# Kernel optimization log

Measured on AMD Instinct MI355X. Metric: run time of the kernel, lower is better.

## Reference

```python
import jax, jax.numpy as jnp
import numpy as np

N_NODES = 100000
N_EDGES = 1600000
IN_DIM = 256
OUT_DIM = 128
EPS = 1e-12  # torch F.normalize default eps


def setup_inputs() -> dict:
    key = jax.random.key(0)
    k1, k2, k3, k4, k5 = jax.random.split(key, 5)
    x = jax.random.normal(k1, (N_NODES, IN_DIM), dtype=jnp.float32)
    edge_index = jax.random.randint(k2, (2, N_EDGES), 0, N_NODES, dtype=jnp.int64)
    # projection (no bias): weight [out, in]
    Wp = jax.random.normal(k3, (OUT_DIM, IN_DIM), dtype=jnp.float32) * 0.05
    # GCNConv internal linear weight [out, out] and output bias [out]
    Wg = jax.random.normal(k4, (OUT_DIM, OUT_DIM), dtype=jnp.float32) * 0.05
    bg = jax.random.normal(k5, (OUT_DIM,), dtype=jnp.float32) * 0.01
    return {"x": x, "edge_index": edge_index, "Wp": Wp, "Wg": Wg, "bg": bg}


def reference(x, edge_index, Wp, Wg, bg):
    n = x.shape[0]
    # projection: x @ Wp^T
    h = x @ Wp.T                      # [N, OUT]
    # GCNConv: transform first, then propagate
    h = h @ Wg.T                      # [N, OUT]
    # add self-loops
    loops = jnp.arange(n, dtype=edge_index.dtype)
    row = jnp.concatenate([edge_index[0], loops])   # source
    col = jnp.concatenate([edge_index[1], loops])   # target
    # symmetric normalization: deg over target index (edge_weight = 1)
    deg = jax.ops.segment_sum(jnp.ones_like(col, dtype=h.dtype), col, num_segments=n)
    dinv = jnp.where(deg > 0, jax.lax.rsqrt(deg), 0.0)
    norm = dinv[row] * dinv[col]                     # [E+N]
    # gather messages from source, scale, scatter-add to target
    msg = h[row] * norm[:, None]                     # [E+N, OUT]
    out = jax.ops.segment_sum(msg, col, num_segments=n)  # [N, OUT]
    out = out + bg
    # F.normalize(dim=1): divide by L2 norm clamped at eps
    nrm = jnp.sqrt(jnp.sum(out * out, axis=1, keepdims=True))
    out = out / jnp.maximum(nrm, EPS)
    return out
```

## Files before the change

### kernel.cpp

```cpp
#include <hip/hip_runtime.h>
#include <hip/hip_fp16.h>

#define NDIM 128
#define KDIM 256
#define MT 5
#define AROW 264
#define CHUNK 3200
#define BSH 8
#define BMASK 255
#define MAXBUCK 400
#define FTH 512

typedef _Float16 half8 __attribute__((ext_vector_type(8)));
typedef _Float16 half4v __attribute__((ext_vector_type(4)));
typedef _Float16 half2v __attribute__((ext_vector_type(2)));
typedef float float4v __attribute__((ext_vector_type(4)));

#if __has_builtin(__builtin_amdgcn_fdot2)
#define HAS_FDOT2 1
#else
#define HAS_FDOT2 0
#endif

__global__ void k_combine_w(const float* __restrict__ Wp, const float* __restrict__ Wg,
                            _Float16* __restrict__ Bfrag) {
    int o = blockIdx.x;
    int i = threadIdx.x;
    float acc = 0.f;
#pragma unroll 4
    for (int k = 0; k < 128; ++k) acc = fmaf(Wg[o * 128 + k], Wp[k * 256 + i], acc);
    int kk = i >> 5, r = i & 31, quad = r >> 3, j = r & 7;
    int ntile = o >> 4, lanen = o & 15, lane = quad * 16 + lanen;
    Bfrag[(((ntile * 8 + kk) * 64) + lane) * 8 + j] = (_Float16)acc;
}

__global__ __launch_bounds__(256) void k_phase1(const int* __restrict__ col, int E,
                                                int* __restrict__ hist, int NBLK, int NBUCK) {
    __shared__ int h[MAXBUCK];
    int tid = threadIdx.x;
    for (int b = tid; b < MAXBUCK; b += 256) h[b] = 0;
    __syncthreads();
    int e0 = blockIdx.x * CHUNK;
    int e1 = min(e0 + CHUNK, E);
    for (int e = e0 + tid; e < e1; e += 256) atomicAdd(&h[col[e] >> BSH], 1);
    __syncthreads();
    for (int b = tid; b < NBUCK; b += 256) hist[b * NBLK + blockIdx.x] = h[b];
}

__global__ __launch_bounds__(1024) void k_scan_blk(int* __restrict__ a, int n,
                                                   int* __restrict__ blockSum) {
    __shared__ int s[1024];
    int t = threadIdx.x;
    int i = blockIdx.x * 1024 + t;
    int v = (i < n) ? a[i] : 0;
    s[t] = v;
    __syncthreads();
    for (int d = 1; d < 1024; d <<= 1) {
        int y = (t >= d) ? s[t - d] : 0;
        __syncthreads();
        s[t] += y;
        __syncthreads();
    }
    if (i < n) a[i] = s[t] - v;
    if (t == 1023) blockSum[blockIdx.x] = s[t];
}

__global__ __launch_bounds__(1024) void k_scan_top(int* __restrict__ blockSum, int nb) {
    __shared__ int s[1024];
    int t = threadIdx.x;
    int v = (t < nb) ? blockSum[t] : 0;
    s[t] = v;
    __syncthreads();
    for (int d = 1; d < 1024; d <<= 1) {
        int y = (t >= d) ? s[t - d] : 0;
        __syncthreads();
        s[t] += y;
        __syncthreads();
    }
    if (t < nb) blockSum[t] = s[t] - v;
}

__global__ __launch_bounds__(256) void k_scan_add(int* __restrict__ a,
                                                  const int* __restrict__ blockOff, int n) {
    int i = blockIdx.x * 256 + threadIdx.x;
    if (i < n) a[i] += blockOff[i >> 10];
}

__global__ __launch_bounds__(256) void k_phase3(const int* __restrict__ ei, int E,
                                                const int* __restrict__ offs, int NBLK, int NBUCK,
                                                int* __restrict__ tmp) {
    __shared__ int cur[MAXBUCK];
    int tid = threadIdx.x;
    for (int b = tid; b < NBUCK; b += 256) cur[b] = offs[b * NBLK + blockIdx.x];
    __syncthreads();
    int e0 = blockIdx.x * CHUNK;
    int e1 = min(e0 + CHUNK, E);
    for (int e = e0 + tid; e < e1; e += 256) {
        int r = ei[e];
        int c = ei[E + e];
        int p = atomicAdd(&cur[c >> BSH], 1);
        tmp[p] = (r << BSH) | (c & BMASK);
    }
}

__global__ __launch_bounds__(FTH) void k_fine(const int* __restrict__ tmp,
                                              const int* __restrict__ offs, int NBLK, int NBUCK,
                                              int N, int E,
                                              int* __restrict__ sortedRow,
                                              int* __restrict__ cnt,
                                              int* __restrict__ rowStart) {
    __shared__ int scnt[256];
    __shared__ int cur[256];
    int b = blockIdx.x;
    int t = threadIdx.x;
    int start = offs[b * NBLK];
    int end = (b + 1 < NBUCK) ? offs[(b + 1) * NBLK] : E;

    if (t < 256) scnt[t] = 0;
    __syncthreads();
    for (int p = start + t; p < end; p += FTH) atomicAdd(&scnt[tmp[p] & BMASK], 1);
    __syncthreads();
    int v = (t < 256) ? scnt[t] : 0;
    for (int d = 1; d < 256; d <<= 1) {
        int y = (t >= d && t < 256) ? scnt[t - d] : 0;
        __syncthreads();
        if (t < 256) scnt[t] += y;
        __syncthreads();
    }
    if (t < 256) {
        int excl = scnt[t] - v;
        int node = (b << BSH) + t;
        if (node < N) {
            cnt[node] = v;
            rowStart[node] = start + excl;
        }
        cur[t] = start + excl;
    }
    __syncthreads();
    for (int p = start + t; p < end; p += FTH) {
        int pr = tmp[p];
        int slot = atomicAdd(&cur[pr & BMASK], 1);
        sortedRow[slot] = pr >> BSH;
    }
    if (b == NBUCK - 1 && t == 0) rowStart[N] = E;
}

__global__ __launch_bounds__(256) void k_gemm_mfma(const float* __restrict__ x,
                                                   const _Float16* __restrict__ Bfrag,
                                                   const int* __restrict__ cnt,
                                                   _Float16* __restrict__ g, int nrows) {
    __shared__ __align__(16) _Float16 xs[2][16 * AROW];
    int tid  = threadIdx.x;
    int lane = tid & 63;
    int w    = tid >> 6;
    int quad = lane >> 4;
    int lcol = lane & 15;

    const half8* Bv = (const half8*)Bfrag;
    half8 b0[8], b1[8];
#pragma unroll
    for (int kk = 0; kk < 8; ++kk) {
        b0[kk] = Bv[(w * 8 + kk) * 64 + lane];
        b1[kk] = Bv[((w + 4) * 8 + kk) * 64 + lane];
    }

    long base = (long)blockIdx.x * (16 * MT);
    for (int t = 0; t < MT; ++t) {
        long m0 = base + t * 16;
        _Float16* xb = xs[t & 1];
        const float4* xv = (const float4*)(x + m0 * KDIM);
#pragma unroll
        for (int ii = 0; ii < 4; ++ii) {
            int idx = tid + ii * 256;
            int m = idx >> 6, k4 = idx & 63;
            float4 v = xv[idx];
            half4v hv = { (_Float16)v.x, (_Float16)v.y, (_Float16)v.z, (_Float16)v.w };
            *(half4v*)&xb[m * AROW + k4 * 4] = hv;
        }
        __syncthreads();

        float4v acc0 = {0.f, 0.f, 0.f, 0.f}, acc1 = {0.f, 0.f, 0.f, 0.f};
#pragma unroll
        for (int kk = 0; kk < 8; ++kk) {
            half8 a = *(const half8*)(&xb[lcol * AROW + kk * 32 + quad * 8]);
            acc0 = __builtin_amdgcn_mfma_f32_16x16x32_f16(a, b0[kk], acc0, 0, 0, 0);
            acc1 = __builtin_amdgcn_mfma_f32_16x16x32_f16(a, b1[kk], acc1, 0, 0, 0);
        }

#pragma unroll
        for (int r = 0; r < 4; ++r) {
            long node = m0 + quad * 4 + r;
            float di = rsqrtf((float)(cnt[node] + 1));
            g[node * NDIM + w * 16 + lcol]        = (_Float16)(acc0[r] * di);
            g[node * NDIM + (w + 4) * 16 + lcol]  = (_Float16)(acc1[r] * di);
        }
    }
}

__global__ __launch_bounds__(256) void k_gather(const _Float16* __restrict__ g,
                                                const int* __restrict__ rowStart,
                                                const int* __restrict__ sortedRow,
                                                const int* __restrict__ cnt,
                                                const float* __restrict__ bg,
                                                float* __restrict__ out) {
    int lane = threadIdx.x & 63;
    int i = blockIdx.x * 4 + (threadIdx.x >> 6);
    const int s = rowStart[i];
    const int e = rowStart[i + 1];
    const int g4  = lane >> 4;
    const int r16 = lane & 15;

    const half8* __restrict__ gv = (const half8*)g;

    float acc[8];
#pragma unroll
    for (int j = 0; j < 8; ++j) acc[j] = 0.f;

#if HAS_FDOT2
    const half2v one2 = { (_Float16)1.0f, (_Float16)1.0f };
#endif

    int p = s;
    for (; p + 16 <= e; p += 16) {
        int r0 = sortedRow[p + g4];
        int r1 = sortedRow[p + 4 + g4];
        int r2 = sortedRow[p + 8 + g4];
        int r3 = sortedRow[p + 12 + g4];
        half8 v0 = gv[(size_t)r0 * 16 + r16];
        half8 v1 = gv[(size_t)r1 * 16 + r16];
        half8 v2 = gv[(size_t)r2 * 16 + r16];
        half8 v3 = gv[(size_t)r3 * 16 + r16];
#if HAS_FDOT2
#pragma unroll
        for (int j = 0; j < 8; ++j) {
            half2v a = { v0[j], v1[j] };
            half2v b = { v2[j], v3[j] };
            acc[j] = __builtin_amdgcn_fdot2(a, one2,
                     __builtin_amdgcn_fdot2(b, one2, acc[j], false), false);
        }
#else
#pragma unroll
        for (int j = 0; j < 8; ++j)
            acc[j] += ((float)v0[j] + (float)v1[j]) + ((float)v2[j] + (float)v3[j]);
#endif
    }
    if (p + 8 <= e) {
        int r0 = sortedRow[p + g4];
        int r1 = sortedRow[p + 4 + g4];
        half8 v0 = gv[(size_t)r0 * 16 + r16];
        half8 v1 = gv[(size_t)r1 * 16 + r16];
#if HAS_FDOT2
#pragma unroll
        for (int j = 0; j < 8; ++j) {
            half2v a = { v0[j], v1[j] };
            acc[j] = __builtin_amdgcn_fdot2(a, one2, acc[j], false);
        }
#else
#pragma unroll
        for (int j = 0; j < 8; ++j) acc[j] += (float)v0[j] + (float)v1[j];
#endif
        p += 8;
    }
    if (p + 4 <= e) {
        int r0 = sortedRow[p + g4];
        half8 v0 = gv[(size_t)r0 * 16 + r16];
#pragma unroll
        for (int j = 0; j < 8; ++j) acc[j] += (float)v0[j];
        p += 4;
    }
    if (p + g4 < e) {
        int r0 = sortedRow[p + g4];
        half8 v0 = gv[(size_t)r0 * 16 + r16];
#pragma unroll
        for (int j = 0; j < 8; ++j) acc[j] += (float)v0[j];
    }

#pragma unroll
    for (int j = 0; j < 8; ++j) {
        acc[j] += __shfl_xor(acc[j], 16);
        acc[j] += __shfl_xor(acc[j], 32);
    }

    half8 sv = gv[(size_t)i * 16 + r16];
#pragma unroll
    for (int j = 0; j < 8; ++j) acc[j] += (float)sv[j];

    float di = rsqrtf((float)(cnt[i] + 1));
    float4 b0 = ((const float4*)bg)[r16 * 2];
    float4 b1 = ((const float4*)bg)[r16 * 2 + 1];
    float v[8];
    v[0] = fmaf(di, acc[0], b0.x);
    v[1] = fmaf(di, acc[1], b0.y);
    v[2] = fmaf(di, acc[2], b0.z);
    v[3] = fmaf(di, acc[3], b0.w);
    v[4] = fmaf(di, acc[4], b1.x);
    v[5] = fmaf(di, acc[5], b1.y);
    v[6] = fmaf(di, acc[6], b1.z);
    v[7] = fmaf(di, acc[7], b1.w);

    float sq = 0.f;
#pragma unroll
    for (int j = 0; j < 8; ++j) sq += v[j] * v[j];
    sq += __shfl_xor(sq, 1);
    sq += __shfl_xor(sq, 2);
    sq += __shfl_xor(sq, 4);
    sq += __shfl_xor(sq, 8);
    float scale = 1.0f / fmaxf(sqrtf(sq), 1e-12f);

    if (g4 == 0) {
        float4 o0 = make_float4(v[0] * scale, v[1] * scale, v[2] * scale, v[3] * scale);
        float4 o1 = make_float4(v[4] * scale, v[5] * scale, v[6] * scale, v[7] * scale);
        ((float4*)out)[(size_t)i * 32 + r16 * 2]     = o0;
        ((float4*)out)[(size_t)i * 32 + r16 * 2 + 1] = o1;
    }
}

extern "C" void kernel_launch(void* const* d_in, const int* in_sizes, int n_in,
                              void* d_out, int out_size, void* d_ws, size_t ws_size,
                              hipStream_t stream) {
    const float* x  = (const float*)d_in[0];
    const int*   ei = (const int*)  d_in[1];
    const float* Wp = (const float*)d_in[2];
    const float* Wg = (const float*)d_in[3];
    const float* bg = (const float*)d_in[4];
    float* out = (float*)d_out;

    const int N = in_sizes[0] / KDIM;
    const int E = in_sizes[1] / 2;

    const int NBLK  = (E + CHUNK - 1) / CHUNK;
    const int NBUCK = (N + BMASK) >> BSH;
    const int NE    = NBLK * NBUCK;
    const int NSB   = (NE + 1023) >> 10;

    char* p = (char*)d_ws;
    auto carve = [&](size_t bytes) { void* r = (void*)p; p += (bytes + 255) & ~(size_t)255; return r; };
    _Float16* g      = (_Float16*)carve((size_t)N * NDIM * 2);
    int*   sortedRow = (int*)  carve((size_t)E * 4);
    int*   tmp       = (int*)  carve((size_t)E * 4);
    _Float16* Bfrag  = (_Float16*)carve((size_t)KDIM * NDIM * 2);
    int*   cnt       = (int*)  carve((size_t)N * 4);
    int*   rowStart  = (int*)  carve((size_t)(N + 1) * 4);
    int*   hist      = (int*)  carve((size_t)NE * 4);
    int*   blockSum  = (int*)  carve((size_t)1024 * 4);

    hipLaunchKernelGGL(k_combine_w, dim3(NDIM), dim3(KDIM), 0, stream, Wp, Wg, Bfrag);
    hipLaunchKernelGGL(k_phase1, dim3(NBLK), dim3(256), 0, stream, ei + E, E, hist, NBLK, NBUCK);
    hipLaunchKernelGGL(k_scan_blk, dim3(NSB), dim3(1024), 0, stream, hist, NE, blockSum);
    hipLaunchKernelGGL(k_scan_top, dim3(1), dim3(1024), 0, stream, blockSum, NSB);
    hipLaunchKernelGGL(k_scan_add, dim3((NE + 255) / 256), dim3(256), 0, stream, hist, blockSum, NE);
    hipLaunchKernelGGL(k_phase3, dim3(NBLK), dim3(256), 0, stream, ei, E, hist, NBLK, NBUCK, tmp);
    hipLaunchKernelGGL(k_fine, dim3(NBUCK), dim3(FTH), 0, stream, tmp, hist, NBLK, NBUCK, N, E,
                       sortedRow, cnt, rowStart);
    hipLaunchKernelGGL(k_gemm_mfma, dim3(N / (16 * MT)), dim3(256), 0, stream, x, Bfrag, cnt, g, N);
    hipLaunchKernelGGL(k_gather, dim3(N / 4), dim3(256), 0, stream,
                       g, rowStart, sortedRow, cnt, bg, out);
}
```

Before: 313.2 us.

## Merge weight combine with histogram, single-pass lookback scan, wider buckets, LDS-cached fine sort

Weight combination and the bucket histogram now run as one launch, split by block index. The three-kernel scan becomes a single kernel in which each block publishes its total with a flag and sums its predecessors' totals by spinning on them. Buckets widen to 512 nodes, so there are fewer buckets and fewer histogram entries. The fine-sort kernel caches each bucket's entries in LDS to avoid reading global memory twice. The gains come from fewer launches and less global traffic, at the cost of a spin-wait that relies on all scan blocks being co-resident and lower occupancy in the fine-sort kernel from its large LDS array.

Result: faster. 296.6 us (-5.3%).

```diff
diff --git a/kernel.cpp b/kernel.cpp
--- a/kernel.cpp
+++ b/kernel.cpp
@@ -6,10 +6,12 @@
 #define MT 5
 #define AROW 264
 #define CHUNK 3200
-#define BSH 8
-#define BMASK 255
-#define MAXBUCK 400
+#define BSH 9
+#define BMASK 511
+#define MAXBUCK 256
 #define FTH 512
+#define ECAP 12032
+#define SFLAG 0x40000000
 
 typedef _Float16 half8 __attribute__((ext_vector_type(8)));
 typedef _Float16 half4v __attribute__((ext_vector_type(4)));
@@ -22,36 +24,45 @@
 #define HAS_FDOT2 0
 #endif
 
-__global__ void k_combine_w(const float* __restrict__ Wp, const float* __restrict__ Wg,
-                            _Float16* __restrict__ Bfrag) {
-    int o = blockIdx.x;
-    int i = threadIdx.x;
-    float acc = 0.f;
-#pragma unroll 4
-    for (int k = 0; k < 128; ++k) acc = fmaf(Wg[o * 128 + k], Wp[k * 256 + i], acc);
-    int kk = i >> 5, r = i & 31, quad = r >> 3, j = r & 7;
-    int ntile = o >> 4, lanen = o & 15, lane = quad * 16 + lanen;
-    Bfrag[(((ntile * 8 + kk) * 64) + lane) * 8 + j] = (_Float16)acc;
-}
-
-__global__ __launch_bounds__(256) void k_phase1(const int* __restrict__ col, int E,
-                                                int* __restrict__ hist, int NBLK, int NBUCK) {
+__global__ __launch_bounds__(256) void k_prep(const float* __restrict__ Wp,
+                                              const float* __restrict__ Wg,
+                                              _Float16* __restrict__ Bfrag,
+                                              const int* __restrict__ ei, int E,
+                                              int* __restrict__ hist, int NBLK, int NBUCK,
+                                              int* __restrict__ partials, int NSB) {
     __shared__ int h[MAXBUCK];
     int tid = threadIdx.x;
-    for (int b = tid; b < MAXBUCK; b += 256) h[b] = 0;
-    __syncthreads();
-    int e0 = blockIdx.x * CHUNK;
-    int e1 = min(e0 + CHUNK, E);
-    for (int e = e0 + tid; e < e1; e += 256) atomicAdd(&h[col[e] >> BSH], 1);
-    __syncthreads();
-    for (int b = tid; b < NBUCK; b += 256) hist[b * NBLK + blockIdx.x] = h[b];
-}
-
-__global__ __launch_bounds__(1024) void k_scan_blk(int* __restrict__ a, int n,
-                                                   int* __restrict__ blockSum) {
+    int blk = blockIdx.x;
+    if (blk < NBLK) {
+        if (blk == 0 && tid < 128) {
+            partials[tid] = 0;
+        }
+        const int* __restrict__ col = ei + E;
+        h[tid] = 0;
+        __syncthreads();
+        int e0 = blk * CHUNK;
+        int e1 = min(e0 + CHUNK, E);
+        for (int e = e0 + tid; e < e1; e += 256) atomicAdd(&h[col[e] >> BSH], 1);
+        __syncthreads();
+        if (tid < NBUCK) hist[tid * NBLK + blk] = h[tid];
+    } else {
+        int o = blk - NBLK;
+        int i = tid;
+        float acc = 0.f;
+#pragma unroll 4
+        for (int k = 0; k < 128; ++k) acc = fmaf(Wg[o * 128 + k], Wp[k * 256 + i], acc);
+        int kk = i >> 5, r = i & 31, quad = r >> 3, j = r & 7;
+        int ntile = o >> 4, lanen = o & 15, lane = quad * 16 + lanen;
+        Bfrag[(((ntile * 8 + kk) * 64) + lane) * 8 + j] = (_Float16)acc;
+    }
+}
+
+__global__ __launch_bounds__(1024) void k_scan_lb(int* __restrict__ a, int n,
+                                                  int* __restrict__ partials) {
     __shared__ int s[1024];
     int t = threadIdx.x;
-    int i = blockIdx.x * 1024 + t;
+    int blk = blockIdx.x;
+    int i = blk * 1024 + t;
     int v = (i < n) ? a[i] : 0;
     s[t] = v;
     __syncthreads();
@@ -61,29 +72,29 @@
         s[t] += y;
         __syncthreads();
     }
-    if (i < n) a[i] = s[t] - v;
-    if (t == 1023) blockSum[blockIdx.x] = s[t];
-}
-
-__global__ __launch_bounds__(1024) void k_scan_top(int* __restrict__ blockSum, int nb) {
-    __shared__ int s[1024];
-    int t = threadIdx.x;
-    int v = (t < nb) ? blockSum[t] : 0;
-    s[t] = v;
-    __syncthreads();
-    for (int d = 1; d < 1024; d <<= 1) {
-        int y = (t >= d) ? s[t - d] : 0;
-        __syncthreads();
-        s[t] += y;
-        __syncthreads();
-    }
-    if (t < nb) blockSum[t] = s[t] - v;
-}
-
-__global__ __launch_bounds__(256) void k_scan_add(int* __restrict__ a,
-                                                  const int* __restrict__ blockOff, int n) {
-    int i = blockIdx.x * 256 + threadIdx.x;
-    if (i < n) a[i] += blockOff[i >> 10];
+    int myincl = s[t];
+    int total = s[1023];
+    if (t == 0)
+        __hip_atomic_store(&partials[blk], total | SFLAG,
+                           __ATOMIC_RELEASE, __HIP_MEMORY_SCOPE_AGENT);
+    int contrib = 0;
+    if (t < blk) {
+        int pv;
+        do {
+            pv = __hip_atomic_load(&partials[t], __ATOMIC_ACQUIRE,
+                                   __HIP_MEMORY_SCOPE_AGENT);
+        } while (!(pv & SFLAG));
+        contrib = pv & ~SFLAG;
+    }
+    __syncthreads();
+    s[t] = contrib;
+    __syncthreads();
+    for (int d = 512; d > 0; d >>= 1) {
+        if (t < d) s[t] += s[t + d];
+        __syncthreads();
+    }
+    int excl = s[0];
+    if (i < n) a[i] = myincl - v + excl;
 }
 
 __global__ __launch_bounds__(256) void k_phase3(const int* __restrict__ ei, int E,
@@ -91,7 +102,7 @@
                                                 int* __restrict__ tmp) {
     __shared__ int cur[MAXBUCK];
     int tid = threadIdx.x;
-    for (int b = tid; b < NBUCK; b += 256) cur[b] = offs[b * NBLK + blockIdx.x];
+    if (tid < NBUCK) cur[tid] = offs[tid * NBLK + blockIdx.x];
     __syncthreads();
     int e0 = blockIdx.x * CHUNK;
     int e1 = min(e0 + CHUNK, E);
@@ -103,31 +114,37 @@
     }
 }
 
-__global__ __launch_bounds__(FTH) void k_fine(const int* __restrict__ tmp,
-                                              const int* __restrict__ offs, int NBLK, int NBUCK,
-                                              int N, int E,
-                                              int* __restrict__ sortedRow,
-                                              int* __restrict__ cnt,
-                                              int* __restrict__ rowStart) {
-    __shared__ int scnt[256];
-    __shared__ int cur[256];
+__global__ __launch_bounds__(FTH, 1) void k_fine(const int* __restrict__ tmp,
+                                                 const int* __restrict__ offs, int NBLK, int NBUCK,
+                                                 int N, int E,
+                                                 int* __restrict__ sortedRow,
+                                                 int* __restrict__ cnt,
+                                                 int* __restrict__ rowStart) {
+    __shared__ int scnt[512];
+    __shared__ int cur[512];
+    __shared__ int ec[ECAP];
     int b = blockIdx.x;
     int t = threadIdx.x;
     int start = offs[b * NBLK];
     int end = (b + 1 < NBUCK) ? offs[(b + 1) * NBLK] : E;
-
-    if (t < 256) scnt[t] = 0;
-    __syncthreads();
-    for (int p = start + t; p < end; p += FTH) atomicAdd(&scnt[tmp[p] & BMASK], 1);
-    __syncthreads();
-    int v = (t < 256) ? scnt[t] : 0;
-    for (int d = 1; d < 256; d <<= 1) {
-        int y = (t >= d && t < 256) ? scnt[t - d] : 0;
-        __syncthreads();
-        if (t < 256) scnt[t] += y;
-        __syncthreads();
-    }
-    if (t < 256) {
+    int len = end - start;
+
+    scnt[t] = 0;
+    __syncthreads();
+    if (len <= ECAP) {
+        for (int p = t; p < len; p += FTH) {
+            int v = tmp[start + p];
+            ec[p] = v;
+            atomicAdd(&scnt[v & BMASK], 1);
+        }
+        __syncthreads();
+        int v = scnt[t];
+        for (int d = 1; d < 512; d <<= 1) {
+            int y = (t >= d) ? scnt[t - d] : 0;
+            __syncthreads();
+            scnt[t] += y;
+            __syncthreads();
+        }
         int excl = scnt[t] - v;
         int node = (b << BSH) + t;
         if (node < N) {
@@ -135,12 +152,35 @@
             rowStart[node] = start + excl;
         }
         cur[t] = start + excl;
-    }
-    __syncthreads();
-    for (int p = start + t; p < end; p += FTH) {
-        int pr = tmp[p];
-        int slot = atomicAdd(&cur[pr & BMASK], 1);
-        sortedRow[slot] = pr >> BSH;
+        __syncthreads();
+        for (int p = t; p < len; p += FTH) {
+            int pr = ec[p];
+            int slot = atomicAdd(&cur[pr & BMASK], 1);
+            sortedRow[slot] = pr >> BSH;
+        }
+    } else {
+        for (int p = start + t; p < end; p += FTH) atomicAdd(&scnt[tmp[p] & BMASK], 1);
+        __syncthreads();
+        int v = scnt[t];
+        for (int d = 1; d < 512; d <<= 1) {
+            int y = (t >= d) ? scnt[t - d] : 0;
+            __syncthreads();
+            scnt[t] += y;
+            __syncthreads();
+        }
+        int excl = scnt[t] - v;
+        int node = (b << BSH) + t;
+        if (node < N) {
+            cnt[node] = v;
+            rowStart[node] = start + excl;
+        }
+        cur[t] = start + excl;
+        __syncthreads();
+        for (int p = start + t; p < end; p += FTH) {
+            int pr = tmp[p];
+            int slot = atomicAdd(&cur[pr & BMASK], 1);
+            sortedRow[slot] = pr >> BSH;
+        }
     }
     if (b == NBUCK - 1 && t == 0) rowStart[N] = E;
 }
@@ -342,13 +382,11 @@
     int*   cnt       = (int*)  carve((size_t)N * 4);
     int*   rowStart  = (int*)  carve((size_t)(N + 1) * 4);
     int*   hist      = (int*)  carve((size_t)NE * 4);
-    int*   blockSum  = (int*)  carve((size_t)1024 * 4);
-
-    hipLaunchKernelGGL(k_combine_w, dim3(NDIM), dim3(KDIM), 0, stream, Wp, Wg, Bfrag);
-    hipLaunchKernelGGL(k_phase1, dim3(NBLK), dim3(256), 0, stream, ei + E, E, hist, NBLK, NBUCK);
-    hipLaunchKernelGGL(k_scan_blk, dim3(NSB), dim3(1024), 0, stream, hist, NE, blockSum);
-    hipLaunchKernelGGL(k_scan_top, dim3(1), dim3(1024), 0, stream, blockSum, NSB);
-    hipLaunchKernelGGL(k_scan_add, dim3((NE + 255) / 256), dim3(256), 0, stream, hist, blockSum, NE);
+    int*   partials  = (int*)  carve((size_t)128 * 4);
+
+    hipLaunchKernelGGL(k_prep, dim3(NBLK + 128), dim3(256), 0, stream,
+                       Wp, Wg, Bfrag, ei, E, hist, NBLK, NBUCK, partials, NSB);
+    hipLaunchKernelGGL(k_scan_lb, dim3(NSB), dim3(1024), 0, stream, hist, NE, partials);
     hipLaunchKernelGGL(k_phase3, dim3(NBLK), dim3(256), 0, stream, ei, E, hist, NBLK, NBUCK, tmp);
     hipLaunchKernelGGL(k_fine, dim3(NBUCK), dim3(FTH), 0, stream, tmp, hist, NBLK, NBUCK, N, E,
                        sortedRow, cnt, rowStart);
```
